# Optimization experiments

Measured on AMD Instinct MI355X. Metric: run time of the kernel, lower is better.

Reference implementation:

```python
import jax, jax.numpy as jnp
import numpy as np

N_HEADS = 12

def setup_inputs() -> dict:
    key = jax.random.key(0)
    k1, k2, k3 = jax.random.split(key, 3)
    B, L, D = 2, 2048, 768
    x = jax.random.normal(k1, (B, L, D), dtype=jnp.float32)
    attention_mask = jnp.ones((B, L), dtype=jnp.int32)  # 1 = real token
    w_qkv = jax.random.normal(k2, (D, 3 * D), dtype=jnp.float32) * (1.0 / np.sqrt(D))
    b_qkv = jnp.zeros((3 * D,), dtype=jnp.float32)
    w_out = jax.random.normal(k3, (D, D), dtype=jnp.float32) * (1.0 / np.sqrt(D))
    b_out = jnp.zeros((D,), dtype=jnp.float32)
    return {"x": x, "attention_mask": attention_mask, "w_qkv": w_qkv,
            "b_qkv": b_qkv, "w_out": w_out, "b_out": b_out}

def reference(x, attention_mask, w_qkv, b_qkv, w_out, b_out):
    B, L, D = x.shape
    H = N_HEADS
    dk = D // H
    # fused QKV projection
    qkv = jnp.einsum('bld,de->ble', x, w_qkv) + b_qkv  # (B,L,3D)
    q, k, v = jnp.split(qkv, 3, axis=-1)
    def to_heads(t):
        return t.reshape(B, L, H, dk).transpose(0, 2, 1, 3)  # (B,H,L,dk)
    q, k, v = to_heads(q), to_heads(k), to_heads(v)
    scale = 1.0 / jnp.sqrt(jnp.asarray(dk, dtype=x.dtype))
    scores = jnp.einsum('bhqd,bhkd->bhqk', q, k) * scale  # (B,H,L,L)
    mask = (attention_mask != 0)[:, None, None, :]  # (B,1,1,L), True = keep
    neg = jnp.asarray(jnp.finfo(scores.dtype).min, dtype=scores.dtype)
    scores = jnp.where(mask, scores, neg)
    weights = jax.nn.softmax(scores, axis=-1)
    out = jnp.einsum('bhqk,bhkd->bhqd', weights, v)  # (B,H,L,dk)
    out = out.transpose(0, 2, 1, 3).reshape(B, L, D)
    return jnp.einsum('bld,de->ble', out, w_out) + b_out
```

## Files before the change

kernel.cpp:

```cpp
#include <hip/hip_runtime.h>

typedef __bf16 bf16;
typedef bf16 bf16x4 __attribute__((ext_vector_type(4)));
typedef bf16 bf16x8 __attribute__((ext_vector_type(8)));
typedef float f32x4 __attribute__((ext_vector_type(4)));

#define MFMA16(A, B, C) __builtin_amdgcn_mfma_f32_16x16x32_bf16(A, B, C, 0, 0, 0)
#define NEG_BIG -30000.0f

#define GLOAD_LDS16(gptr, lptr)                                                \
    __builtin_amdgcn_global_load_lds(                                          \
        (__attribute__((address_space(1))) void*)(gptr),                       \
        (__attribute__((address_space(3))) void*)(lptr), 16, 0, 0)

#define SW(r, c8) ((r) * 64 + (((((c8) >> 3) ^ ((r) & 7))) << 3))
#define SW32(r, q) ((r) * 32 + ((((q) ^ ((r) & 3))) << 3))

__global__ void mark_k(float* __restrict__ out, float val, int n) {
    int i = blockIdx.x * 256 + threadIdx.x;
    if (i < n) out[i] = val;
}

__global__ __launch_bounds__(256) void cvt_x_k(const float* __restrict__ src,
                                               bf16* __restrict__ dst, int n) {
    int i = (blockIdx.x * 256 + threadIdx.x) * 8;
    if (i >= n) return;
    float4 a = *(const float4*)&src[i];
    float4 b = *(const float4*)&src[i + 4];
    bf16x8 w;
    w[0] = (bf16)a.x; w[1] = (bf16)a.y; w[2] = (bf16)a.z; w[3] = (bf16)a.w;
    w[4] = (bf16)b.x; w[5] = (bf16)b.y; w[6] = (bf16)b.z; w[7] = (bf16)b.w;
    *(bf16x8*)&dst[i] = w;
}

__global__ __launch_bounds__(256) void transpose_cvt_tiled(
    const float* __restrict__ src, bf16* __restrict__ dst, int R, int C) {
    __shared__ float t[32][33];
    int tid = threadIdx.x, tx = tid & 31, ty = tid >> 5;
    int bx = blockIdx.x * 32, by = blockIdx.y * 32;
#pragma unroll
    for (int i = 0; i < 4; ++i) {
        int row = by + ty + i * 8;
        t[ty + i * 8][tx] = src[(size_t)row * C + bx + tx];
    }
    __syncthreads();
#pragma unroll
    for (int i = 0; i < 4; ++i) {
        int outrow = bx + ty + i * 8;
        dst[(size_t)outrow * R + by + tx] = (bf16)t[tx][ty + i * 8];
    }
}

#define CLD 136

__global__ __launch_bounds__(256) void gemm_qkv_v5(
    const bf16* __restrict__ A, const bf16* __restrict__ B,
    const float* __restrict__ bias, bf16* __restrict__ Qh,
    bf16* __restrict__ Kh, bf16* __restrict__ Vth) {
    __shared__ __align__(16) bf16 SMEM[128 * CLD];
    int tid = threadIdx.x, lane = tid & 63, wave = tid >> 6;
    int quad = lane >> 4, l16 = lane & 15;
    int wr = wave >> 1, wc = wave & 1;
    int m0 = blockIdx.y * 128, n0 = blockIdx.x * 128;
    const int K = 768;
    const f32x4 fz = {0.f, 0.f, 0.f, 0.f};
    f32x4 acc[4][4];
#pragma unroll
    for (int nj = 0; nj < 4; ++nj)
#pragma unroll
        for (int mi = 0; mi < 4; ++mi) acc[nj][mi] = fz;
    const bf16* Ablk = A + (size_t)m0 * K;
    const bf16* Bblk = B + (size_t)n0 * K;

    int srow = lane >> 2;
    int c    = lane & 3;

#pragma unroll
    for (int i = 0; i < 2; ++i) {
        int r0 = i * 64 + wave * 16;
        int row = r0 + srow;
        int sc = (c ^ (row & 3)) << 3;
        GLOAD_LDS16(&Ablk[(size_t)row * K + sc], &SMEM[r0 * 32]);
        GLOAD_LDS16(&Bblk[(size_t)row * K + sc], &SMEM[4096 + r0 * 32]);
    }

    int p = 0;
    for (int k0 = 0; k0 < K; k0 += 32) {
        __syncthreads();

        if (k0 + 32 < K) {
            int kn = k0 + 32;
#pragma unroll
            for (int i = 0; i < 2; ++i) {
                int r0 = i * 64 + wave * 16;
                int row = r0 + srow;
                int sc = (c ^ (row & 3)) << 3;
                GLOAD_LDS16(&Ablk[(size_t)row * K + kn + sc],
                            &SMEM[(1 - p) * 8192 + r0 * 32]);
                GLOAD_LDS16(&Bblk[(size_t)row * K + kn + sc],
                            &SMEM[4096 + (1 - p) * 8192 + r0 * 32]);
            }
        }

        const bf16* Asp = &SMEM[p * 8192];
        const bf16* Bsp = &SMEM[4096 + p * 8192];
        bf16x8 af[4], bfv[4];
#pragma unroll
        for (int t = 0; t < 4; ++t) {
            af[t]  = *(const bf16x8*)&Asp[SW32(wr * 64 + t * 16 + l16, quad)];
            bfv[t] = *(const bf16x8*)&Bsp[SW32(wc * 64 + t * 16 + l16, quad)];
        }
#pragma unroll
        for (int nj = 0; nj < 4; ++nj)
#pragma unroll
            for (int mi = 0; mi < 4; ++mi)
                acc[nj][mi] = MFMA16(bfv[nj], af[mi], acc[nj][mi]);
        p ^= 1;
    }

    int which = n0 / 768;
    int h0 = (n0 % 768) >> 6;
    int b = m0 >> 11, l0 = m0 & 2047;
    __syncthreads();

    if (which == 2) {
#pragma unroll
        for (int nj = 0; nj < 4; ++nj) {
            int cl0 = wc * 64 + nj * 16 + quad * 4;
            float4 bv4 = *(const float4*)&bias[n0 + cl0];
            float bv[4] = {bv4.x, bv4.y, bv4.z, bv4.w};
#pragma unroll
            for (int mi = 0; mi < 4; ++mi) {
                int xrl = wr * 64 + mi * 16 + l16;
#pragma unroll
                for (int r = 0; r < 4; ++r)
                    SMEM[(cl0 + r) * CLD + xrl] = (bf16)(acc[nj][mi][r] + bv[r]);
            }
        }
    } else {
        float s = (which == 0) ? 0.125f : 1.0f;
#pragma unroll
        for (int nj = 0; nj < 4; ++nj) {
            int cl0 = wc * 64 + nj * 16 + quad * 4;
            float4 bv4 = *(const float4*)&bias[n0 + cl0];
            float bv[4] = {bv4.x, bv4.y, bv4.z, bv4.w};
#pragma unroll
            for (int mi = 0; mi < 4; ++mi) {
                int xrl = wr * 64 + mi * 16 + l16;
                bf16x4 v;
#pragma unroll
                for (int r = 0; r < 4; ++r) v[r] = (bf16)((acc[nj][mi][r] + bv[r]) * s);
                *(bf16x4*)&SMEM[xrl * CLD + cl0] = v;
            }
        }
    }
    __syncthreads();

    if (which == 2) {
#pragma unroll
        for (int i = 0; i < 8; ++i) {
            int idx = i * 256 + tid;
            int cl = idx >> 4, ch = idx & 15;
            int d = cl & 63, h = h0 + (cl >> 6);
            bf16x8 v = *(const bf16x8*)&SMEM[cl * CLD + ch * 8];
            *(bf16x8*)&Vth[((size_t)(b * 12 + h) * 64 + d) * 2048 + l0 + ch * 8] = v;
        }
    } else {
        bf16* dst = (which == 0) ? Qh : Kh;
#pragma unroll
        for (int i = 0; i < 8; ++i) {
            int idx = i * 256 + tid;
            int rr = idx >> 4, ch = idx & 15;
            int h = h0 + (ch >> 3), d0 = (ch & 7) * 8;
            bf16x8 v = *(const bf16x8*)&SMEM[rr * CLD + ch * 8];
            *(bf16x8*)&dst[((size_t)(b * 12 + h) * 2048 + l0 + rr) * 64 + d0] = v;
        }
    }
}

__global__ __launch_bounds__(128) void gemm_out_v4(
    const bf16* __restrict__ A, const bf16* __restrict__ B,
    const float* __restrict__ bias, float* __restrict__ C) {
    __shared__ __align__(16) bf16 As[2][128 * 32];
    __shared__ __align__(16) bf16 Bs[2][64 * 32];
    int tid = threadIdx.x, lane = tid & 63, wave = tid >> 6;
    int quad = lane >> 4, l16 = lane & 15;
    int m0 = blockIdx.y * 128, n0 = blockIdx.x * 64;
    const int K = 768, N = 768;
    const f32x4 fz = {0.f, 0.f, 0.f, 0.f};
    f32x4 acc[4][4];
#pragma unroll
    for (int mi = 0; mi < 4; ++mi)
#pragma unroll
        for (int nj = 0; nj < 4; ++nj) acc[mi][nj] = fz;
    const bf16* Ablk = A + (size_t)m0 * K;
    const bf16* Bblk = B + (size_t)n0 * K;
    int srow = lane >> 2, c = lane & 3;

#pragma unroll
    for (int i = 0; i < 4; ++i) {
        int r0 = i * 32 + wave * 16;
        int row = r0 + srow;
        int sc = (c ^ (row & 3)) << 3;
        GLOAD_LDS16(&Ablk[(size_t)row * K + sc], &As[0][r0 * 32]);
    }
#pragma unroll
    for (int i = 0; i < 2; ++i) {
        int r0 = i * 32 + wave * 16;
        int row = r0 + srow;
        int sc = (c ^ (row & 3)) << 3;
        GLOAD_LDS16(&Bblk[(size_t)row * K + sc], &Bs[0][r0 * 32]);
    }

    int p = 0;
    for (int k0 = 0; k0 < K; k0 += 32) {
        __syncthreads();

        if (k0 + 32 < K) {
            int kn = k0 + 32;
#pragma unroll
            for (int i = 0; i < 4; ++i) {
                int r0 = i * 32 + wave * 16;
                int row = r0 + srow;
                int sc = (c ^ (row & 3)) << 3;
                GLOAD_LDS16(&Ablk[(size_t)row * K + kn + sc], &As[1 - p][r0 * 32]);
            }
#pragma unroll
            for (int i = 0; i < 2; ++i) {
                int r0 = i * 32 + wave * 16;
                int row = r0 + srow;
                int sc = (c ^ (row & 3)) << 3;
                GLOAD_LDS16(&Bblk[(size_t)row * K + kn + sc], &Bs[1 - p][r0 * 32]);
            }
        }

        bf16x8 af[4], bfv[4];
#pragma unroll
        for (int t = 0; t < 4; ++t) {
            af[t]  = *(const bf16x8*)&As[p][SW32(wave * 64 + t * 16 + l16, quad)];
            bfv[t] = *(const bf16x8*)&Bs[p][SW32(t * 16 + l16, quad)];
        }
#pragma unroll
        for (int mi = 0; mi < 4; ++mi)
#pragma unroll
            for (int nj = 0; nj < 4; ++nj)
                acc[mi][nj] = MFMA16(af[mi], bfv[nj], acc[mi][nj]);
        p ^= 1;
    }

#pragma unroll
    for (int nj = 0; nj < 4; ++nj) {
        int col = n0 + nj * 16 + l16;
        float bv = bias[col];
#pragma unroll
        for (int mi = 0; mi < 4; ++mi)
#pragma unroll
            for (int r = 0; r < 4; ++r) {
                int row = m0 + wave * 64 + mi * 16 + quad * 4 + r;
                C[(size_t)row * N + col] = acc[mi][nj][r] + bv;
            }
    }
}

#define PLD 72

__global__ __launch_bounds__(256) void flash_attn(
    const bf16* __restrict__ Q, const bf16* __restrict__ K,
    const bf16* __restrict__ V, const int* __restrict__ mask,
    bf16* __restrict__ ctx) {
    __shared__ __align__(16) bf16 Ks[2][64 * 64];
    __shared__ __align__(16) bf16 Vs[2][64 * 64];
    __shared__ __align__(16) bf16 Ps[4][16 * PLD];
    __shared__ float maskS[2048];
    __shared__ int cleanF;

    int tid = threadIdx.x, lane = tid & 63, wave = tid >> 6;
    int quad = lane >> 4, l16 = lane & 15;
    int bh = blockIdx.y, b = bh / 12;
    int q0 = blockIdx.x * 128 + wave * 32;

    bf16x8 aq[2][2];
#pragma unroll
    for (int qt = 0; qt < 2; ++qt) {
        const bf16* Qp = Q + ((size_t)bh * 2048 + q0 + qt * 16 + l16) * 64;
        aq[qt][0] = *(const bf16x8*)(Qp + quad * 8);
        aq[qt][1] = *(const bf16x8*)(Qp + 32 + quad * 8);
    }

    if (tid == 0) cleanF = 1;
    __syncthreads();
    const int* mrow = mask + b * 2048;
    int myclean = 1;
#pragma unroll
    for (int i = 0; i < 8; ++i) {
        int idx = i * 256 + tid;
        int mv = mrow[idx];
        maskS[idx] = mv ? 0.0f : NEG_BIG;
        myclean &= (mv != 0);
    }
    if (!myclean) cleanF = 0;

    const f32x4 fz = {0.f, 0.f, 0.f, 0.f};
    f32x4 o[2][4];
    float m_i[2], l_i[2];
#pragma unroll
    for (int qt = 0; qt < 2; ++qt) {
        m_i[qt] = NEG_BIG; l_i[qt] = 0.f;
#pragma unroll
        for (int dt = 0; dt < 4; ++dt) o[qt][dt] = fz;
    }

    int srow = tid >> 3;
    int sc8  = (tid & 7) * 8;
    const bf16* Kbase = K + (size_t)bh * 2048 * 64;
    const bf16* Vbase = V + (size_t)bh * 64 * 2048;

#pragma unroll
    for (int i = 0; i < 2; ++i) {
        int row = srow + i * 32;
        *(bf16x8*)&Ks[0][SW(row, sc8)] =
            *(const bf16x8*)&Kbase[(size_t)row * 64 + sc8];
        *(bf16x8*)&Vs[0][SW(row, sc8)] =
            *(const bf16x8*)&Vbase[(size_t)row * 2048 + sc8];
    }
    __syncthreads();
    int clean = cleanF;

    int p = 0;
    for (int kb = 0; kb < 2048; kb += 64) {
        __syncthreads();

        if (kb + 64 < 2048) {
            int nb = kb + 64;
#pragma unroll
            for (int i = 0; i < 2; ++i) {
                int row = srow + i * 32;
                *(bf16x8*)&Ks[1 - p][SW(row, sc8)] =
                    *(const bf16x8*)&Kbase[(size_t)(nb + row) * 64 + sc8];
                *(bf16x8*)&Vs[1 - p][SW(row, sc8)] =
                    *(const bf16x8*)&Vbase[(size_t)row * 2048 + nb + sc8];
            }
        }

        f32x4 s[2][4];
#pragma unroll
        for (int ct = 0; ct < 4; ++ct) {
            int krow = ct * 16 + l16;
            bf16x8 kf0 = *(const bf16x8*)&Ks[p][SW(krow, quad * 8)];
            bf16x8 kf1 = *(const bf16x8*)&Ks[p][SW(krow, 32 + quad * 8)];
#pragma unroll
            for (int qt = 0; qt < 2; ++qt) {
                f32x4 t = fz;
                t = MFMA16(kf0, aq[qt][0], t);
                t = MFMA16(kf1, aq[qt][1], t);
                s[qt][ct] = t;
            }
        }

        if (!clean) {
#pragma unroll
            for (int ct = 0; ct < 4; ++ct) {
                const float* mk = &maskS[kb + ct * 16 + quad * 4];
                float4 mv = *(const float4*)mk;
                float ma[4] = {mv.x, mv.y, mv.z, mv.w};
#pragma unroll
                for (int qt = 0; qt < 2; ++qt)
#pragma unroll
                    for (int r = 0; r < 4; ++r) s[qt][ct][r] += ma[r];
            }
        }

        float alpha[2];
#pragma unroll
        for (int qt = 0; qt < 2; ++qt) {
            float mx = NEG_BIG;
#pragma unroll
            for (int ct = 0; ct < 4; ++ct)
#pragma unroll
                for (int r = 0; r < 4; ++r) mx = fmaxf(mx, s[qt][ct][r]);
            mx = fmaxf(mx, __shfl_xor(mx, 16));
            mx = fmaxf(mx, __shfl_xor(mx, 32));
            float nm = fmaxf(m_i[qt], mx);
            alpha[qt] = __expf(m_i[qt] - nm);
            m_i[qt] = nm;
            float sum = 0.f;
#pragma unroll
            for (int ct = 0; ct < 4; ++ct)
#pragma unroll
                for (int r = 0; r < 4; ++r) {
                    float pv = __expf(s[qt][ct][r] - nm);
                    s[qt][ct][r] = pv;
                    sum += pv;
                }
            sum += __shfl_xor(sum, 16);
            sum += __shfl_xor(sum, 32);
            l_i[qt] = l_i[qt] * alpha[qt] + sum;
        }

#pragma unroll
        for (int qt = 0; qt < 2; ++qt) {
            float ab[4];
#pragma unroll
            for (int r = 0; r < 4; ++r)
                ab[r] = __shfl(alpha[qt], (lane & 48) | (quad * 4 + r));
#pragma unroll
            for (int dt = 0; dt < 4; ++dt)
#pragma unroll
                for (int r = 0; r < 4; ++r) o[qt][dt][r] *= ab[r];
        }

        bf16x8 vf[2][4];
#pragma unroll
        for (int ks = 0; ks < 2; ++ks)
#pragma unroll
            for (int dt = 0; dt < 4; ++dt)
                vf[ks][dt] = *(const bf16x8*)&Vs[p][SW(dt * 16 + l16, ks * 32 + quad * 8)];

#pragma unroll
        for (int qt = 0; qt < 2; ++qt) {
#pragma unroll
            for (int ct = 0; ct < 4; ++ct) {
                bf16x4 pk;
#pragma unroll
                for (int r = 0; r < 4; ++r) pk[r] = (bf16)s[qt][ct][r];
                *(bf16x4*)&Ps[wave][l16 * PLD + ct * 16 + quad * 4] = pk;
            }
#pragma unroll
            for (int ks = 0; ks < 2; ++ks) {
                bf16x8 ap = *(const bf16x8*)&Ps[wave][l16 * PLD + ks * 32 + quad * 8];
#pragma unroll
                for (int dt = 0; dt < 4; ++dt)
                    o[qt][dt] = MFMA16(ap, vf[ks][dt], o[qt][dt]);
            }
        }
        p ^= 1;
    }

    int h = bh % 12;
#pragma unroll
    for (int qt = 0; qt < 2; ++qt) {
        float linv[4];
#pragma unroll
        for (int r = 0; r < 4; ++r)
            linv[r] = 1.0f / __shfl(l_i[qt], (lane & 48) | (quad * 4 + r));
#pragma unroll
        for (int dt = 0; dt < 4; ++dt)
#pragma unroll
            for (int r = 0; r < 4; ++r) {
                int qrow = q0 + qt * 16 + quad * 4 + r;
                ctx[((size_t)b * 2048 + qrow) * 768 + h * 64 + dt * 16 + l16] =
                    (bf16)(o[qt][dt][r] * linv[r]);
            }
    }
}

extern "C" void kernel_launch(void* const* d_in, const int* in_sizes, int n_in,
                              void* d_out, int out_size, void* d_ws, size_t ws_size,
                              hipStream_t stream) {
    float* out = (float*)d_out;

    const float* x = nullptr; const int* mask = nullptr;
    const float* w_qkv = nullptr; const float* b_qkv = nullptr;
    const float* w_out = nullptr; const float* b_out = nullptr;
    int found = 0;
    for (int i = 0; i < n_in; ++i) {
        switch (in_sizes[i]) {
            case 3145728: x     = (const float*)d_in[i]; found |= 1;  break;
            case 4096:    mask  = (const int*)  d_in[i]; found |= 2;  break;
            case 1769472: w_qkv = (const float*)d_in[i]; found |= 4;  break;
            case 2304:    b_qkv = (const float*)d_in[i]; found |= 8;  break;
            case 589824:  w_out = (const float*)d_in[i]; found |= 16; break;
            case 768:     b_out = (const float*)d_in[i]; found |= 32; break;
        }
    }
    if (found != 63) {
        mark_k<<<(out_size + 255) / 256, 256, 0, stream>>>(
            out, 200.0f + (float)found, out_size);
        return;
    }

    const int M = 4096, D = 768, N3 = 2304;
    const size_t HEADS_ELEMS = (size_t)24 * 2048 * 64;

    bf16* ws    = (bf16*)d_ws;
    bf16* Kh    = ws;
    bf16* Vth   = Kh + HEADS_ELEMS;
    bf16* ctx   = Vth + HEADS_ELEMS;
    bf16* wqkvT = ctx + (size_t)M * D;
    bf16* woutT = wqkvT + (size_t)N3 * D;
    bf16* Qh    = (bf16*)d_out;
    bf16* xb    = (bf16*)d_out + HEADS_ELEMS;

    cvt_x_k<<<(M * D / 8 + 255) / 256, 256, 0, stream>>>(x, xb, M * D);
    transpose_cvt_tiled<<<dim3(2304 / 32, 768 / 32), 256, 0, stream>>>(
        w_qkv, wqkvT, 768, 2304);
    transpose_cvt_tiled<<<dim3(768 / 32, 768 / 32), 256, 0, stream>>>(
        w_out, woutT, 768, 768);

    gemm_qkv_v5<<<dim3(N3 / 128, M / 128), 256, 0, stream>>>(
        xb, wqkvT, b_qkv, Qh, Kh, Vth);

    flash_attn<<<dim3(2048 / 128, 24), 256, 0, stream>>>(Qh, Kh, Vth, mask, ctx);

    gemm_out_v4<<<dim3(D / 64, M / 128), 128, 0, stream>>>(
        ctx, woutT, b_out, out);
}
```

Measured before the change: 200.6 us.

## Widen flash-attention KV tile to 128 and drop double buffering

The flash attention kernel now processes 128 keys per iteration instead of 64, using single-buffered K and V shared tiles with a new 128-wide swizzle for V. Global-to-shared loads are no longer prefetched into a second buffer. Instead each iteration loads, synchronizes, then computes. This halves the number of softmax rescale steps and loop barriers per query tile, but it gives up the overlap of loads with compute and increases register pressure from the larger score array.

```diff
diff --git a/kernel.cpp b/kernel.cpp
--- a/kernel.cpp
+++ b/kernel.cpp
@@ -14,6 +14,7 @@
         (__attribute__((address_space(3))) void*)(lptr), 16, 0, 0)
 
 #define SW(r, c8) ((r) * 64 + (((((c8) >> 3) ^ ((r) & 7))) << 3))
+#define SW128(r, c) ((r) * 128 + ((((c) ^ ((r) & 15))) << 3))
 #define SW32(r, q) ((r) * 32 + ((((q) ^ ((r) & 3))) << 3))
 
 __global__ void mark_k(float* __restrict__ out, float val, int n) {
@@ -71,9 +72,7 @@
         for (int mi = 0; mi < 4; ++mi) acc[nj][mi] = fz;
     const bf16* Ablk = A + (size_t)m0 * K;
     const bf16* Bblk = B + (size_t)n0 * K;
-
-    int srow = lane >> 2;
-    int c    = lane & 3;
+    int srow = lane >> 2, c = lane & 3;
 
 #pragma unroll
     for (int i = 0; i < 2; ++i) {
@@ -87,7 +86,6 @@
     int p = 0;
     for (int k0 = 0; k0 < K; k0 += 32) {
         __syncthreads();
-
         if (k0 + 32 < K) {
             int kn = k0 + 32;
 #pragma unroll
@@ -101,7 +99,6 @@
                             &SMEM[4096 + (1 - p) * 8192 + r0 * 32]);
             }
         }
-
         const bf16* Asp = &SMEM[p * 8192];
         const bf16* Bsp = &SMEM[4096 + p * 8192];
         bf16x8 af[4], bfv[4];
@@ -215,7 +212,6 @@
     int p = 0;
     for (int k0 = 0; k0 < K; k0 += 32) {
         __syncthreads();
-
         if (k0 + 32 < K) {
             int kn = k0 + 32;
 #pragma unroll
@@ -233,7 +229,6 @@
                 GLOAD_LDS16(&Bblk[(size_t)row * K + kn + sc], &Bs[1 - p][r0 * 32]);
             }
         }
-
         bf16x8 af[4], bfv[4];
 #pragma unroll
         for (int t = 0; t < 4; ++t) {
@@ -268,8 +263,8 @@
     const bf16* __restrict__ Q, const bf16* __restrict__ K,
     const bf16* __restrict__ V, const int* __restrict__ mask,
     bf16* __restrict__ ctx) {
-    __shared__ __align__(16) bf16 Ks[2][64 * 64];
-    __shared__ __align__(16) bf16 Vs[2][64 * 64];
+    __shared__ __align__(16) bf16 Ks[128 * 64];
+    __shared__ __align__(16) bf16 Vs[64 * 128];
     __shared__ __align__(16) bf16 Ps[4][16 * PLD];
     __shared__ float maskS[2048];
     __shared__ int cleanF;
@@ -310,44 +305,35 @@
         for (int dt = 0; dt < 4; ++dt) o[qt][dt] = fz;
     }
 
-    int srow = tid >> 3;
-    int sc8  = (tid & 7) * 8;
     const bf16* Kbase = K + (size_t)bh * 2048 * 64;
     const bf16* Vbase = V + (size_t)bh * 64 * 2048;
-
-#pragma unroll
-    for (int i = 0; i < 2; ++i) {
-        int row = srow + i * 32;
-        *(bf16x8*)&Ks[0][SW(row, sc8)] =
-            *(const bf16x8*)&Kbase[(size_t)row * 64 + sc8];
-        *(bf16x8*)&Vs[0][SW(row, sc8)] =
-            *(const bf16x8*)&Vbase[(size_t)row * 2048 + sc8];
-    }
     __syncthreads();
     int clean = cleanF;
 
-    int p = 0;
-    for (int kb = 0; kb < 2048; kb += 64) {
+    for (int kb = 0; kb < 2048; kb += 128) {
         __syncthreads();
-
-        if (kb + 64 < 2048) {
-            int nb = kb + 64;
-#pragma unroll
-            for (int i = 0; i < 2; ++i) {
-                int row = srow + i * 32;
-                *(bf16x8*)&Ks[1 - p][SW(row, sc8)] =
-                    *(const bf16x8*)&Kbase[(size_t)(nb + row) * 64 + sc8];
-                *(bf16x8*)&Vs[1 - p][SW(row, sc8)] =
-                    *(const bf16x8*)&Vbase[(size_t)row * 2048 + nb + sc8];
-            }
-        }
-
-        f32x4 s[2][4];
-#pragma unroll
-        for (int ct = 0; ct < 4; ++ct) {
+#pragma unroll
+        for (int i = 0; i < 4; ++i) {
+            int idx = i * 256 + tid;
+            {
+                int row = idx >> 3, c8 = (idx & 7) * 8;
+                *(bf16x8*)&Ks[SW(row, c8)] =
+                    *(const bf16x8*)&Kbase[(size_t)(kb + row) * 64 + c8];
+            }
+            {
+                int row = idx >> 4, cc = idx & 15;
+                *(bf16x8*)&Vs[SW128(row, cc)] =
+                    *(const bf16x8*)&Vbase[(size_t)row * 2048 + kb + cc * 8];
+            }
+        }
+        __syncthreads();
+
+        f32x4 s[2][8];
+#pragma unroll
+        for (int ct = 0; ct < 8; ++ct) {
             int krow = ct * 16 + l16;
-            bf16x8 kf0 = *(const bf16x8*)&Ks[p][SW(krow, quad * 8)];
-            bf16x8 kf1 = *(const bf16x8*)&Ks[p][SW(krow, 32 + quad * 8)];
+            bf16x8 kf0 = *(const bf16x8*)&Ks[SW(krow, quad * 8)];
+            bf16x8 kf1 = *(const bf16x8*)&Ks[SW(krow, 32 + quad * 8)];
 #pragma unroll
             for (int qt = 0; qt < 2; ++qt) {
                 f32x4 t = fz;
@@ -359,9 +345,8 @@
 
         if (!clean) {
 #pragma unroll
-            for (int ct = 0; ct < 4; ++ct) {
-                const float* mk = &maskS[kb + ct * 16 + quad * 4];
-                float4 mv = *(const float4*)mk;
+            for (int ct = 0; ct < 8; ++ct) {
+                float4 mv = *(const float4*)&maskS[kb + ct * 16 + quad * 4];
                 float ma[4] = {mv.x, mv.y, mv.z, mv.w};
 #pragma unroll
                 for (int qt = 0; qt < 2; ++qt)
@@ -375,7 +360,7 @@
         for (int qt = 0; qt < 2; ++qt) {
             float mx = NEG_BIG;
 #pragma unroll
-            for (int ct = 0; ct < 4; ++ct)
+            for (int ct = 0; ct < 8; ++ct)
 #pragma unroll
                 for (int r = 0; r < 4; ++r) mx = fmaxf(mx, s[qt][ct][r]);
             mx = fmaxf(mx, __shfl_xor(mx, 16));
@@ -385,7 +370,7 @@
             m_i[qt] = nm;
             float sum = 0.f;
 #pragma unroll
-            for (int ct = 0; ct < 4; ++ct)
+            for (int ct = 0; ct < 8; ++ct)
 #pragma unroll
                 for (int r = 0; r < 4; ++r) {
                     float pv = __expf(s[qt][ct][r] - nm);
@@ -409,31 +394,29 @@
                 for (int r = 0; r < 4; ++r) o[qt][dt][r] *= ab[r];
         }
 
-        bf16x8 vf[2][4];
-#pragma unroll
-        for (int ks = 0; ks < 2; ++ks)
-#pragma unroll
-            for (int dt = 0; dt < 4; ++dt)
-                vf[ks][dt] = *(const bf16x8*)&Vs[p][SW(dt * 16 + l16, ks * 32 + quad * 8)];
-
 #pragma unroll
         for (int qt = 0; qt < 2; ++qt) {
 #pragma unroll
-            for (int ct = 0; ct < 4; ++ct) {
-                bf16x4 pk;
-#pragma unroll
-                for (int r = 0; r < 4; ++r) pk[r] = (bf16)s[qt][ct][r];
-                *(bf16x4*)&Ps[wave][l16 * PLD + ct * 16 + quad * 4] = pk;
-            }
-#pragma unroll
-            for (int ks = 0; ks < 2; ++ks) {
-                bf16x8 ap = *(const bf16x8*)&Ps[wave][l16 * PLD + ks * 32 + quad * 8];
-#pragma unroll
-                for (int dt = 0; dt < 4; ++dt)
-                    o[qt][dt] = MFMA16(ap, vf[ks][dt], o[qt][dt]);
-            }
-        }
-        p ^= 1;
+            for (int hh = 0; hh < 2; ++hh) {
+#pragma unroll
+                for (int ct = 0; ct < 4; ++ct) {
+                    bf16x4 pk;
+#pragma unroll
+                    for (int r = 0; r < 4; ++r) pk[r] = (bf16)s[qt][hh * 4 + ct][r];
+                    *(bf16x4*)&Ps[wave][l16 * PLD + ct * 16 + quad * 4] = pk;
+                }
+#pragma unroll
+                for (int ks = 0; ks < 2; ++ks) {
+                    bf16x8 ap = *(const bf16x8*)&Ps[wave][l16 * PLD + ks * 32 + quad * 8];
+#pragma unroll
+                    for (int dt = 0; dt < 4; ++dt) {
+                        bf16x8 vf = *(const bf16x8*)&Vs[SW128(dt * 16 + l16,
+                                                              hh * 8 + ks * 4 + quad)];
+                        o[qt][dt] = MFMA16(ap, vf, o[qt][dt]);
+                    }
+                }
+            }
+        }
     }
 
     int h = bh % 12;
```

Result: slower. 232.1 us (+15.7%).

## Split attention over two key halves and merge partial results

Applied to the files above, without the earlier changes.

Flash attention now runs a third grid dimension of two key splits, each covering 1024 keys. Each split writes unnormalized partial outputs plus per-row max and sum statistics. A new merge kernel rescales and combines the two partials into the context buffer. The aim is to double the block count so work spreads more evenly across CUs. The cost is an extra launch and extra memory traffic, and partial outputs are rounded to bf16 before merging.

```diff
diff --git a/kernel.cpp b/kernel.cpp
--- a/kernel.cpp
+++ b/kernel.cpp
@@ -71,9 +71,7 @@
         for (int mi = 0; mi < 4; ++mi) acc[nj][mi] = fz;
     const bf16* Ablk = A + (size_t)m0 * K;
     const bf16* Bblk = B + (size_t)n0 * K;
-
-    int srow = lane >> 2;
-    int c    = lane & 3;
+    int srow = lane >> 2, c = lane & 3;
 
 #pragma unroll
     for (int i = 0; i < 2; ++i) {
@@ -87,7 +85,6 @@
     int p = 0;
     for (int k0 = 0; k0 < K; k0 += 32) {
         __syncthreads();
-
         if (k0 + 32 < K) {
             int kn = k0 + 32;
 #pragma unroll
@@ -101,7 +98,6 @@
                             &SMEM[4096 + (1 - p) * 8192 + r0 * 32]);
             }
         }
-
         const bf16* Asp = &SMEM[p * 8192];
         const bf16* Bsp = &SMEM[4096 + p * 8192];
         bf16x8 af[4], bfv[4];
@@ -215,7 +211,6 @@
     int p = 0;
     for (int k0 = 0; k0 < K; k0 += 32) {
         __syncthreads();
-
         if (k0 + 32 < K) {
             int kn = k0 + 32;
 #pragma unroll
@@ -233,7 +228,6 @@
                 GLOAD_LDS16(&Bblk[(size_t)row * K + kn + sc], &Bs[1 - p][r0 * 32]);
             }
         }
-
         bf16x8 af[4], bfv[4];
 #pragma unroll
         for (int t = 0; t < 4; ++t) {
@@ -267,16 +261,18 @@
 __global__ __launch_bounds__(256) void flash_attn(
     const bf16* __restrict__ Q, const bf16* __restrict__ K,
     const bf16* __restrict__ V, const int* __restrict__ mask,
-    bf16* __restrict__ ctx) {
+    bf16* __restrict__ po0, bf16* __restrict__ po1, float2* __restrict__ lm2) {
     __shared__ __align__(16) bf16 Ks[2][64 * 64];
     __shared__ __align__(16) bf16 Vs[2][64 * 64];
     __shared__ __align__(16) bf16 Ps[4][16 * PLD];
-    __shared__ float maskS[2048];
+    __shared__ float maskS[1024];
     __shared__ int cleanF;
 
     int tid = threadIdx.x, lane = tid & 63, wave = tid >> 6;
     int quad = lane >> 4, l16 = lane & 15;
     int bh = blockIdx.y, b = bh / 12;
+    int split = blockIdx.z;
+    int s0 = split * 1024;
     int q0 = blockIdx.x * 128 + wave * 32;
 
     bf16x8 aq[2][2];
@@ -289,10 +285,10 @@
 
     if (tid == 0) cleanF = 1;
     __syncthreads();
-    const int* mrow = mask + b * 2048;
+    const int* mrow = mask + b * 2048 + s0;
     int myclean = 1;
 #pragma unroll
-    for (int i = 0; i < 8; ++i) {
+    for (int i = 0; i < 4; ++i) {
         int idx = i * 256 + tid;
         int mv = mrow[idx];
         maskS[idx] = mv ? 0.0f : NEG_BIG;
@@ -312,8 +308,8 @@
 
     int srow = tid >> 3;
     int sc8  = (tid & 7) * 8;
-    const bf16* Kbase = K + (size_t)bh * 2048 * 64;
-    const bf16* Vbase = V + (size_t)bh * 64 * 2048;
+    const bf16* Kbase = K + ((size_t)bh * 2048 + s0) * 64;
+    const bf16* Vbase = V + (size_t)bh * 64 * 2048 + s0;
 
 #pragma unroll
     for (int i = 0; i < 2; ++i) {
@@ -327,10 +323,10 @@
     int clean = cleanF;
 
     int p = 0;
-    for (int kb = 0; kb < 2048; kb += 64) {
+    for (int kb = 0; kb < 1024; kb += 64) {
         __syncthreads();
 
-        if (kb + 64 < 2048) {
+        if (kb + 64 < 1024) {
             int nb = kb + 64;
 #pragma unroll
             for (int i = 0; i < 2; ++i) {
@@ -360,8 +356,7 @@
         if (!clean) {
 #pragma unroll
             for (int ct = 0; ct < 4; ++ct) {
-                const float* mk = &maskS[kb + ct * 16 + quad * 4];
-                float4 mv = *(const float4*)mk;
+                float4 mv = *(const float4*)&maskS[kb + ct * 16 + quad * 4];
                 float ma[4] = {mv.x, mv.y, mv.z, mv.w};
 #pragma unroll
                 for (int qt = 0; qt < 2; ++qt)
@@ -437,21 +432,47 @@
     }
 
     int h = bh % 12;
+    bf16* obase = split ? po1 : po0;
 #pragma unroll
     for (int qt = 0; qt < 2; ++qt) {
-        float linv[4];
-#pragma unroll
-        for (int r = 0; r < 4; ++r)
-            linv[r] = 1.0f / __shfl(l_i[qt], (lane & 48) | (quad * 4 + r));
 #pragma unroll
         for (int dt = 0; dt < 4; ++dt)
 #pragma unroll
             for (int r = 0; r < 4; ++r) {
                 int qrow = q0 + qt * 16 + quad * 4 + r;
-                ctx[((size_t)b * 2048 + qrow) * 768 + h * 64 + dt * 16 + l16] =
-                    (bf16)(o[qt][dt][r] * linv[r]);
-            }
-    }
+                obase[((size_t)b * 2048 + qrow) * 768 + h * 64 + dt * 16 + l16] =
+                    (bf16)o[qt][dt][r];
+            }
+        if (quad == 0) {
+            int qrow = q0 + qt * 16 + l16;
+            lm2[((size_t)split * 24 + bh) * 2048 + qrow] =
+                make_float2(m_i[qt], l_i[qt]);
+        }
+    }
+}
+
+__global__ __launch_bounds__(256) void merge_k(
+    bf16* __restrict__ ctx , const bf16* __restrict__ po1,
+    const float2* __restrict__ lm2) {
+    int idx = blockIdx.x * 256 + threadIdx.x;
+    if (idx >= 4096 * 768 / 8) return;
+    size_t i8 = (size_t)idx * 8;
+    int row = (int)(i8 / 768);
+    int col = (int)(i8 % 768);
+    int bh = (row >> 11) * 12 + (col >> 6);
+    int qrow = row & 2047;
+    float2 a = lm2[(size_t)bh * 2048 + qrow];
+    float2 c = lm2[(size_t)(24 + bh) * 2048 + qrow];
+    float m = fmaxf(a.x, c.x);
+    float w0 = __expf(a.x - m), w1 = __expf(c.x - m);
+    float inv = 1.0f / (a.y * w0 + c.y * w1);
+    bf16x8 v0 = *(const bf16x8*)&ctx[i8];
+    bf16x8 v1 = *(const bf16x8*)&po1[i8];
+    bf16x8 o;
+#pragma unroll
+    for (int k = 0; k < 8; ++k)
+        o[k] = (bf16)(((float)v0[k] * w0 + (float)v1[k] * w1) * inv);
+    *(bf16x8*)&ctx[i8] = o;
 }
 
 extern "C" void kernel_launch(void* const* d_in, const int* in_sizes, int n_in,
@@ -490,6 +511,8 @@
     bf16* woutT = wqkvT + (size_t)N3 * D;
     bf16* Qh    = (bf16*)d_out;
     bf16* xb    = (bf16*)d_out + HEADS_ELEMS;
+    bf16* po1   = xb;
+    float2* lm2 = (float2*)wqkvT;
 
     cvt_x_k<<<(M * D / 8 + 255) / 256, 256, 0, stream>>>(x, xb, M * D);
     transpose_cvt_tiled<<<dim3(2304 / 32, 768 / 32), 256, 0, stream>>>(
@@ -500,7 +523,10 @@
     gemm_qkv_v5<<<dim3(N3 / 128, M / 128), 256, 0, stream>>>(
         xb, wqkvT, b_qkv, Qh, Kh, Vth);
 
-    flash_attn<<<dim3(2048 / 128, 24), 256, 0, stream>>>(Qh, Kh, Vth, mask, ctx);
+    flash_attn<<<dim3(2048 / 128, 24, 2), 256, 0, stream>>>(
+        Qh, Kh, Vth, mask, ctx, po1, lm2);
+
+    merge_k<<<(4096 * 768 / 8 + 255) / 256, 256, 0, stream>>>(ctx, po1, lm2);
 
     gemm_out_v4<<<dim3(D / 64, M / 128), 128, 0, stream>>>(
         ctx, woutT, b_out, out);
```

Measured after the change: 195.9 us. -2.3%, faster.
